# Optimization experiments

Measured on AMD Instinct MI355X. Metric: run time of the kernel, lower is better.

## Reference

```python
import jax, jax.numpy as jnp
from jax import lax
import numpy as np

# pywt.Wavelet('sym5').dec_lo; true convolution with rec_lo == correlation with dec_lo
_DEC_LO = jnp.array([0.027333068345077982, 0.029519490925774643, -0.039134249302383094,
                     0.1993975339773936, 0.7234076904024206, 0.6339789634582119,
                     0.01660210576452232, -0.17532808990845047, -0.021101834024758855,
                     0.019538882735286728], dtype=jnp.float32)
_KERNEL = _DEC_LO[None, None, :]  # (O=1, I=1, L=10)


def _idwt_approx(c):
    # One inverse-DWT level with zero detail coeffs.
    # pywt idwt: upsample by 2, full conv with rec_lo, slice [L-2 : L-2 + 2n-L+2].
    # Equivalent: lhs_dilation=2, padding=(1,1), correlation with dec_lo.
    B, n = c.shape
    out = lax.conv_general_dilated(c[:, None, :], _KERNEL, window_strides=(1,),
                                   padding=[(1, 1)], lhs_dilation=(2,),
                                   dimension_numbers=('NCH', 'OIH', 'NCH'))
    return out[:, 0, :]  # (B, 2n - 8)


def _waverec3(cA):
    # waverec with coeffs [cA(20), zeros(20), zeros(31), zeros(54)], sym5 -> length 100
    a = _idwt_approx(cA)      # 20 -> 32
    a = a[:, :31]             # pywt waverec crops a to len(d)=31
    a = _idwt_approx(a)       # 31 -> 54
    a = _idwt_approx(a)       # 54 -> 100
    return a


def _ce(logits, target):
    logp = jax.nn.log_softmax(logits, axis=-1)
    return -jnp.take_along_axis(logp, target[:, None], axis=-1)[:, 0]


def _ohem(logits, target, train_mask, ratio=3.0):
    ce = _ce(logits, target)
    tf = target.astype(jnp.float32)
    pos = (tf * train_mask) > 0
    neg = ((1.0 - tf) * train_mask) > 0
    n_pos = jnp.sum(pos.astype(jnp.float32))
    count_neg = jnp.sum(neg.astype(jnp.float32))
    loss_pos = jnp.where(n_pos > 0, jnp.sum(jnp.where(pos, ce, 0.0)), 0.0)
    n_neg = jnp.where(n_pos > 0, jnp.minimum(count_neg, jnp.floor(ratio * n_pos)), 100.0)
    srt = jnp.sort(jnp.where(neg, ce, -jnp.inf))[::-1]
    take = (jnp.arange(srt.shape[0]) < n_neg) & jnp.isfinite(srt)
    loss_neg = jnp.sum(jnp.where(take, srt, 0.0))
    return (loss_pos + loss_neg) / (n_pos + n_neg)


def _smooth_l1(d):
    ad = jnp.abs(d)
    return jnp.where(ad < 1.0, 0.5 * d * d, ad - 0.5)


def _forward_single(cls_pred, reg_pred, gt):
    cp = jnp.transpose(cls_pred, (0, 2, 3, 1)).reshape(-1, 4)
    rp = jnp.transpose(reg_pred, (0, 2, 3, 1)).reshape(-1, 42)
    g = jnp.transpose(gt, (0, 2, 3, 1)).reshape(-1, 45)
    tr_pred, tcl_pred = cp[:, :2], cp[:, 2:]
    wl_r, xc_p, wl_i, yc_p = rp[:, :20], rp[:, 20], rp[:, 21:41], rp[:, 41]
    tr_mask, tcl_mask, train_mask = g[:, 0], g[:, 1], g[:, 2]
    real_g, xc_g, imag_g, yc_g = g[:, 3:23], g[:, 23], g[:, 24:44], g[:, 44]
    ttm = train_mask * tr_mask
    n_pos = jnp.sum(ttm)

    loss_tr = _ohem(tr_pred, tr_mask.astype(jnp.int32), train_mask)

    ce_tcl = _ce(tcl_pred, tcl_mask.astype(jnp.int32))
    neg_m = 1.0 - ttm
    mp = jnp.sum(ce_tcl * ttm) / jnp.maximum(n_pos, 1.0)
    mn = jnp.sum(ce_tcl * neg_m) / jnp.maximum(jnp.sum(neg_m), 1.0)
    loss_tcl = jnp.where(n_pos > 0, mp + 0.5 * mn, 0.0)

    px = _waverec3(wl_r) + xc_p[:, None]   # (M,100)
    py = _waverec3(wl_i) + yc_p[:, None]
    gx = _waverec3(real_g) + xc_g[:, None]
    gy = _waverec3(imag_g) + yc_g[:, None]
    per_pix = jnp.sum(_smooth_l1(px - gx) + _smooth_l1(py - gy), axis=-1)  # (M,)
    loss_contour = jnp.where(n_pos > 0, 0.5 * jnp.sum(ttm * per_pix) / (n_pos * 200.0), 0.0)
    return jnp.stack([loss_tr, loss_tcl, loss_contour])


def setup_inputs() -> dict:
    key = jax.random.key(0)
    N = 8
    out = {}
    for name, H in (("3", 100), ("4", 50), ("5", 25)):
        k1, k2, k3, k4, k5, k6 = jax.random.split(jax.random.fold_in(key, int(name)), 6)
        out["cls" + name] = jax.random.normal(k1, (N, 4, H, H), jnp.float32)
        out["reg" + name] = jax.random.normal(k2, (N, 42, H, H), jnp.float32)
        tr = jax.random.bernoulli(k3, 0.1, (N, 1, H, H)).astype(jnp.float32)
        tcl = jax.random.bernoulli(k4, 0.5, (N, 1, H, H)).astype(jnp.float32)
        train = jax.random.bernoulli(k5, 0.9, (N, 1, H, H)).astype(jnp.float32)
        rest = jax.random.normal(k6, (N, 42, H, H), jnp.float32)
        out["gt" + name] = jnp.concatenate([tr, tcl, train, rest], axis=1)  # 45 ch
    return out


def reference(cls3, reg3, gt3, cls4, reg4, gt4, cls5, reg5, gt5):
    total = (_forward_single(cls3, reg3, gt3)
             + _forward_single(cls4, reg4, gt4)
             + _forward_single(cls5, reg5, gt5))
    return total  # [loss_text, loss_center, loss_contour]
```

## Files before the change

kernel.cpp:

```cpp
#include <hip/hip_runtime.h>
#include <math.h>

#define DEVI __device__ __forceinline__

static constexpr float KD[10] = {
  0.027333068345077982f,  0.029519490925774643f, -0.039134249302383094f,
  0.1993975339773936f,    0.7234076904024206f,    0.6339789634582119f,
  0.01660210576452232f,  -0.17532808990845047f,  -0.021101834024758855f,
  0.019538882735286728f};

#define CE_OFF     0
#define PH_OFF     105056
#define PH1_REL    40192
#define PH2_REL    50432
#define MH_OFF     160608
#define BS_OFF     234336
#define SLOTGT_OFF 308064
#define STATE_OFF  308352
#define SLOT2_OFF  308384
#define CBUF_OFF   308672
#define CAPC       49152
#define PART_OFF   456128
#define PART_STRIDE 3840

#define NB3 157
#define NB4 40
#define NB5 20
#define NBR 96

DEVI float wave_sum(float v) {
#pragma unroll
  for (int d = 32; d; d >>= 1) v += __shfl_down(v, d);
  return v;
}

DEVI float block_sum(float v, float* sh) {
  int lane = threadIdx.x & 63, wid = threadIdx.x >> 6;
  v = wave_sum(v);
  if (lane == 0) sh[wid] = v;
  __syncthreads();
  if (threadIdx.x == 0) {
    float s = 0.f;
    int nw = blockDim.x >> 6;
    for (int w = 0; w < nw; ++w) s += sh[w];
    sh[0] = s;
  }
  __syncthreads();
  float r = sh[0];
  __syncthreads();
  return r;
}

DEVI int suffix_scan_256(int v, int* sh) {
  int t = threadIdx.x;
  sh[t] = v;
  __syncthreads();
#pragma unroll
  for (int off = 1; off < 256; off <<= 1) {
    int x = (t + off < 256) ? sh[t + off] : 0;
    __syncthreads();
    sh[t] += x;
    __syncthreads();
  }
  return sh[t];
}

DEVI float sl1(float v) { float a = fabsf(v); return (a < 1.f) ? 0.5f * v * v : a - 0.5f; }

DEVI float ce2cls(float la, float lb, float tgt) {
  float m = fmaxf(la, lb);
  float lse = m + __logf(__expf(la - m) + __expf(lb - m));
  return lse - ((tgt > 0.5f) ? lb : la);
}

template <int H>
DEVI float recon_half(const float* __restrict__ rb, const float* __restrict__ gb,
                      int rc0, int gc0, size_t HW, float off) {
  constexpr int CLO  = (H == 0) ? 0 : 6;
  constexpr int A1LO = (H == 0) ? 0 : 12;
  constexpr int J2LO = (H == 0) ? 0 : 25;
  float c[14];
#pragma unroll
  for (int i = 0; i < 14; ++i)
    c[i] = rb[(size_t)(rc0 + CLO + i) * HW] - gb[(size_t)(gc0 + CLO + i) * HW];
  float a1[19];
#pragma unroll
  for (int k = 0; k < 19; ++k) {
    int o1 = A1LO + k, b = (o1 >> 1) - CLO;
    if (o1 & 1)
      a1[k] = KD[0]*c[b] + KD[2]*c[b+1] + KD[4]*c[b+2] + KD[6]*c[b+3] + KD[8]*c[b+4];
    else
      a1[k] = KD[1]*c[b] + KD[3]*c[b+1] + KD[5]*c[b+2] + KD[7]*c[b+3] + KD[9]*c[b+4];
  }
  float w0=0.f,w1=0.f,w2=0.f,w3=0.f,w4=0.f, acc=0.f;
#pragma unroll
  for (int k = 0; k < 29; ++k) {
    int j2 = J2LO + k, b = (j2 >> 1) - A1LO;
    float a2v;
    if (j2 & 1)
      a2v = KD[0]*a1[b] + KD[2]*a1[b+1] + KD[4]*a1[b+2] + KD[6]*a1[b+3] + KD[8]*a1[b+4];
    else
      a2v = KD[1]*a1[b] + KD[3]*a1[b+1] + KD[5]*a1[b+2] + KD[7]*a1[b+3] + KD[9]*a1[b+4];
    w0=w1; w1=w2; w2=w3; w3=w4; w4=a2v;
    if (k >= 4) {
      acc += sl1(KD[1]*w0 + KD[3]*w1 + KD[5]*w2 + KD[7]*w3 + KD[9]*w4 + off);
      acc += sl1(KD[0]*w0 + KD[2]*w1 + KD[4]*w2 + KD[6]*w3 + KD[8]*w4 + off);
    }
  }
  return acc;
}

DEVI float2 tap2o(const float2* a, int b) {
  float2 r;
  r.x = KD[0]*a[b].x + KD[2]*a[b+1].x + KD[4]*a[b+2].x + KD[6]*a[b+3].x + KD[8]*a[b+4].x;
  r.y = KD[0]*a[b].y + KD[2]*a[b+1].y + KD[4]*a[b+2].y + KD[6]*a[b+3].y + KD[8]*a[b+4].y;
  return r;
}
DEVI float2 tap2e(const float2* a, int b) {
  float2 r;
  r.x = KD[1]*a[b].x + KD[3]*a[b+1].x + KD[5]*a[b+2].x + KD[7]*a[b+3].x + KD[9]*a[b+4].x;
  r.y = KD[1]*a[b].y + KD[3]*a[b+1].y + KD[5]*a[b+2].y + KD[7]*a[b+3].y + KD[9]*a[b+4].y;
  return r;
}
template <int H>
DEVI float2 recon2(const float* __restrict__ rb, const float* __restrict__ gb,
                   int rc0, int gc0, size_t HW, float2 off) {
  constexpr int CLO  = (H == 0) ? 0 : 6;
  constexpr int A1LO = (H == 0) ? 0 : 12;
  constexpr int J2LO = (H == 0) ? 0 : 25;
  float2 c[14];
#pragma unroll
  for (int i = 0; i < 14; ++i) {
    float2 rv = *(const float2*)(rb + (size_t)(rc0 + CLO + i) * HW);
    float2 gv = *(const float2*)(gb + (size_t)(gc0 + CLO + i) * HW);
    c[i].x = rv.x - gv.x; c[i].y = rv.y - gv.y;
  }
  float2 a1[19];
#pragma unroll
  for (int k = 0; k < 19; ++k) {
    int o1 = A1LO + k, b = (o1 >> 1) - CLO;
    a1[k] = (o1 & 1) ? tap2o(c, b) : tap2e(c, b);
  }
  float2 w0={0,0},w1={0,0},w2={0,0},w3={0,0},w4={0,0};
  float2 acc={0,0};
#pragma unroll
  for (int k = 0; k < 29; ++k) {
    int j2 = J2LO + k, b = (j2 >> 1) - A1LO;
    float2 a2v = (j2 & 1) ? tap2o(a1, b) : tap2e(a1, b);
    w0=w1; w1=w2; w2=w3; w3=w4; w4=a2v;
    if (k >= 4) {
      float vex = KD[1]*w0.x + KD[3]*w1.x + KD[5]*w2.x + KD[7]*w3.x + KD[9]*w4.x + off.x;
      float vey = KD[1]*w0.y + KD[3]*w1.y + KD[5]*w2.y + KD[7]*w3.y + KD[9]*w4.y + off.y;
      float vox = KD[0]*w0.x + KD[2]*w1.x + KD[4]*w2.x + KD[6]*w3.x + KD[8]*w4.x + off.x;
      float voy = KD[0]*w0.y + KD[2]*w1.y + KD[4]*w2.y + KD[6]*w3.y + KD[8]*w4.y + off.y;
      acc.x += sl1(vex) + sl1(vox);
      acc.y += sl1(vey) + sl1(voy);
    }
  }
  return acc;
}

__global__ void __launch_bounds__(256, 3)
pixel_kernel(const float* __restrict__ cls3, const float* __restrict__ reg3, const float* __restrict__ gt3,
             const float* __restrict__ cls4, const float* __restrict__ reg4, const float* __restrict__ gt4,
             const float* __restrict__ cls5, const float* __restrict__ reg5, const float* __restrict__ gt5,
             float* __restrict__ ws, float* __restrict__ out) {
  int bx = blockIdx.x, y = blockIdx.y, t = threadIdx.x;
  int axis = y >> 1, half = y & 1;
  const float *cls, *reg, *gt;
  int M, HW, ceOff, partBase, phRel, nb, lbx, two;
  if (bx < NB3) {
    cls = cls3; reg = reg3; gt = gt3; M = 80000; HW = 10000;
    ceOff = 0; partBase = PART_OFF; phRel = 0; nb = NB3; lbx = bx; two = 1;
  } else if (bx < NB3 + NB4) {
    cls = cls4; reg = reg4; gt = gt4; M = 20000; HW = 2500;
    ceOff = 80000; partBase = PART_OFF + PART_STRIDE; phRel = PH1_REL; nb = NB4; lbx = bx - NB3; two = 1;
  } else {
    cls = cls5; reg = reg5; gt = gt5; M = 5000; HW = 625;
    ceOff = 100000; partBase = PART_OFF + 2 * PART_STRIDE; phRel = PH2_REL; nb = NB5; lbx = bx - NB3 - NB4; two = 0;
  }
  float* ceArr = ws + ceOff;
  unsigned* ph = (unsigned*)(ws + PH_OFF) + phRel;

  if (bx == 0 && y == 0 && t < 3) out[t] = 0.f;

  __shared__ unsigned hlds[256];
  __shared__ float shp[4][6];
  hlds[t] = 0u;
  __syncthreads();

  float cnt_pos = 0.f, cnt_neg = 0.f, s_ce_pos = 0.f, s_tcl_ttm = 0.f, s_tcl_negm = 0.f;
  float s_ttm_pp = 0.f;
  int rc0 = axis ? 21 : 0;
  int gc0 = axis ? 24 : 3;

  if (two) {
    int p0 = (lbx * 256 + t) * 2;
    if (p0 < M) {
      int n = p0 / HW, hw = p0 % HW;
      const float* gb = gt  + (size_t)n * 45 * HW + hw;
      const float* rb = reg + (size_t)n * 42 * HW + hw;
      float2 trv = *(const float2*)(gb);
      float2 tnv = *(const float2*)(gb + 2 * (size_t)HW);
      float2 ttm; ttm.x = trv.x * tnv.x; ttm.y = trv.y * tnv.y;

      if (y == 0) {
        const float* cb = cls + (size_t)n * 4 * HW + hw;
        float2 l0 = *(const float2*)(cb);
        float2 l1 = *(const float2*)(cb + (size_t)HW);
        float2 l2 = *(const float2*)(cb + 2 * (size_t)HW);
        float2 l3 = *(const float2*)(cb + 3 * (size_t)HW);
        float2 tcl = *(const float2*)(gb + (size_t)HW);
        float cex = ce2cls(l0.x, l1.x, trv.x), cey = ce2cls(l0.y, l1.y, trv.y);
        float ctx = ce2cls(l2.x, l3.x, tcl.x), cty = ce2cls(l2.y, l3.y, tcl.y);
        bool posx = ttm.x > 0.f, posy = ttm.y > 0.f;
        bool negx = ((1.f - trv.x) * tnv.x) > 0.f, negy = ((1.f - trv.y) * tnv.y) > 0.f;
        float cvx = negx ? cex : 0.f, cvy = negy ? cey : 0.f;
        float2 cev; cev.x = cvx; cev.y = cvy;
        *(float2*)(ceArr + p0) = cev;
        if (negx) atomicAdd(&hlds[__float_as_uint(cvx) >> 23], 1u);
        if (negy) atomicAdd(&hlds[__float_as_uint(cvy) >> 23], 1u);
        cnt_pos = (posx ? 1.f : 0.f) + (posy ? 1.f : 0.f);
        cnt_neg = (negx ? 1.f : 0.f) + (negy ? 1.f : 0.f);
        s_ce_pos = (posx ? cex : 0.f) + (posy ? cey : 0.f);
        s_tcl_ttm = ctx * ttm.x + cty * ttm.y;
        s_tcl_negm = ctx * (1.f - ttm.x) + cty * (1.f - ttm.y);
      }

      float2 rcv = *(const float2*)(rb + (size_t)(rc0 + 20) * HW);
      float2 gcv = *(const float2*)(gb + (size_t)(gc0 + 20) * HW);
      float2 dc; dc.x = rcv.x - gcv.x; dc.y = rcv.y - gcv.y;
      float2 pp = half ? recon2<1>(rb, gb, rc0, gc0, (size_t)HW, dc)
                       : recon2<0>(rb, gb, rc0, gc0, (size_t)HW, dc);
      s_ttm_pp = ttm.x * pp.x + ttm.y * pp.y;
    }
  } else {
    int p = lbx * 256 + t;
    if (p < M) {
      int n = p / HW, hw = p % HW;
      const float* gb = gt  + (size_t)n * 45 * HW + hw;
      const float* rb = reg + (size_t)n * 42 * HW + hw;
      float tr = gb[0], train = gb[2 * (size_t)HW];
      float ttm = tr * train;
      if (y == 0) {
        const float* cb = cls + (size_t)n * 4 * HW + hw;
        float ce_tr = ce2cls(cb[0], cb[(size_t)HW], tr);
        float ce_tcl = ce2cls(cb[2 * (size_t)HW], cb[3 * (size_t)HW], gb[(size_t)HW]);
        bool pos = ttm > 0.f;
        bool neg = ((1.f - tr) * train) > 0.f;
        float cev = neg ? ce_tr : 0.f;
        ceArr[p] = cev;
        if (neg) atomicAdd(&hlds[__float_as_uint(cev) >> 23], 1u);
        cnt_pos = pos ? 1.f : 0.f;
        cnt_neg = neg ? 1.f : 0.f;
        s_ce_pos = pos ? ce_tr : 0.f;
        s_tcl_ttm = ce_tcl * ttm;
        s_tcl_negm = ce_tcl * (1.f - ttm);
      }
      float dc = rb[(size_t)(rc0 + 20) * HW] - gb[(size_t)(gc0 + 20) * HW];
      float pp = half ? recon_half<1>(rb, gb, rc0, gc0, (size_t)HW, dc)
                      : recon_half<0>(rb, gb, rc0, gc0, (size_t)HW, dc);
      s_ttm_pp = ttm * pp;
    }
  }

  int lane = t & 63, wid = t >> 6;
  cnt_pos = wave_sum(cnt_pos);
  cnt_neg = wave_sum(cnt_neg);
  s_ce_pos = wave_sum(s_ce_pos);
  s_tcl_ttm = wave_sum(s_tcl_ttm);
  s_tcl_negm = wave_sum(s_tcl_negm);
  s_ttm_pp = wave_sum(s_ttm_pp);
  if (lane == 0) {
    shp[wid][0] = cnt_pos; shp[wid][1] = cnt_neg; shp[wid][2] = s_ce_pos;
    shp[wid][3] = s_tcl_ttm; shp[wid][4] = s_tcl_negm; shp[wid][5] = s_ttm_pp;
  }
  __syncthreads();
  if (t < 6) {
    float s = shp[0][t] + shp[1][t] + shp[2][t] + shp[3][t];
    ws[partBase + (size_t)(y * nb + lbx) * 6 + t] = s;
  }
  if (y == 0)
    ph[(size_t)lbx * 256 + t] = hlds[t];
}

__global__ void refine_kernel(float* __restrict__ ws) {
  int s = blockIdx.y, r = blockIdx.x, t = threadIdx.x;
  int M   = (s == 0) ? 80000 : (s == 1 ? 20000 : 5000);
  int off = (s == 0) ? 0     : (s == 1 ? 80000 : 100000);
  int nb0 = (s == 0) ? NB3   : (s == 1 ? NB4   : NB5);
  int phRel = (s == 0) ? 0 : (s == 1 ? PH1_REL : PH2_REL);
  int* st = (int*)(ws + STATE_OFF) + s * 8;

  __shared__ int sh[256];
  __shared__ int sel[2];
  __shared__ float red[4];
  __shared__ unsigned hW[4][256];
  __shared__ unsigned mhL[256];
  __shared__ float bsL[256];

  const float* part = ws + PART_OFF + s * PART_STRIDE;
  int npart = 4 * nb0;
  float a0 = 0.f, a1 = 0.f, a2 = 0.f, a3 = 0.f, a4 = 0.f, a5 = 0.f;
  for (int i = t; i < npart; i += 256) {
    const float* p6 = part + (size_t)i * 6;
    a0 += p6[0]; a1 += p6[1]; a2 += p6[2]; a3 += p6[3]; a4 += p6[4]; a5 += p6[5];
  }
  a0 = block_sum(a0, red);
  a1 = block_sum(a1, red);
  a2 = block_sum(a2, red);
  a3 = block_sum(a3, red);
  a4 = block_sum(a4, red);
  a5 = block_sum(a5, red);

  float cnt_pos = a0, cnt_negf = a1;
  int cnt_neg = (int)cnt_negf;
  float kf = (cnt_pos > 0.f) ? fminf(cnt_negf, floorf(3.f * cnt_pos)) : 100.f;
  int k_take = min((int)kf, cnt_neg);

  int ibin, rem;
  if (k_take >= cnt_neg) { ibin = -1; rem = 0; }
  else if (k_take <= 0)  { ibin = 256; rem = 0; }
  else {
    const uint4* ph4 = (const uint4*)((const unsigned*)(ws + PH_OFF) + phRel);
    unsigned c0 = 0u, c1 = 0u, c2 = 0u, c3 = 0u;
    int n4 = nb0 * 64;
    for (int i = t; i < n4; i += 256) {
      uint4 u = ph4[i];
      c0 += u.x; c1 += u.y; c2 += u.z; c3 += u.w;
    }
    int wid = t >> 6, b0 = (4 * t) & 255;
    hW[wid][b0 + 0] = c0; hW[wid][b0 + 1] = c1; hW[wid][b0 + 2] = c2; hW[wid][b0 + 3] = c3;
    __syncthreads();
    int h = (int)(hW[0][t] + hW[1][t] + hW[2][t] + hW[3][t]);
    int suf = suffix_scan_256(h, sh);
    int above = suf - h;
    if (suf >= k_take && above < k_take) { sel[0] = t; sel[1] = k_take - above; }
    __syncthreads();
    ibin = sel[0]; rem = sel[1];
    __syncthreads();
  }
  if (r == 0 && t == 0) {
    st[0] = ibin; st[1] = rem;
    float* stf = (float*)st;
    stf[2] = kf; stf[3] = a0; stf[4] = a2; stf[5] = a3; stf[6] = a4; stf[7] = a5;
  }

  mhL[t] = 0u; bsL[t] = 0.f;
  __syncthreads();
  const float* ce = ws + off;
  float sum = 0.f;
  for (int i = r * 256 + t; i < M; i += NBR * 256) {
    float v = ce[i];
    unsigned b = __float_as_uint(v);
    int e = (int)(b >> 23);
    if (e > ibin) sum += v;
    else if (e == ibin && rem > 0) {
      int m8 = (int)((b >> 15) & 255u);
      atomicAdd(&mhL[m8], 1u);
      atomicAdd(&bsL[m8], v);
    }
  }
  sum = block_sum(sum, red);
  if (t == 0) ws[SLOTGT_OFF + s * NBR + r] = sum;
  if (rem > 0) {
    ((unsigned*)(ws + MH_OFF))[((size_t)s * NBR + r) * 256 + t] = mhL[t];
    ws[BS_OFF + ((size_t)s * NBR + r) * 256 + t] = bsL[t];
  }
}

__global__ void compactB_kernel(float* __restrict__ ws) {
  int s = blockIdx.y, r = blockIdx.x, t = threadIdx.x;
  int M   = (s == 0) ? 80000 : (s == 1 ? 20000 : 5000);
  int off = (s == 0) ? 0     : (s == 1 ? 80000 : 100000);
  const int* st = (const int*)(ws + STATE_OFF) + s * 8;
  int ibin = st[0], rem = st[1];
  if (rem <= 0) return;

  __shared__ int sh[256];
  __shared__ int sel[2];
  __shared__ float red[4];
  __shared__ unsigned hW[4][256];
  __shared__ unsigned wcnt;

  const unsigned* mh = (const unsigned*)(ws + MH_OFF) + (size_t)s * NBR * 256;
  const uint4* mh4 = (const uint4*)mh;
  unsigned c0 = 0u, c1 = 0u, c2 = 0u, c3 = 0u;
  for (int i = t; i < NBR * 64; i += 256) {
    uint4 u = mh4[i];
    c0 += u.x; c1 += u.y; c2 += u.z; c3 += u.w;
  }
  int wid = t >> 6, b0 = (4 * t) & 255;
  hW[wid][b0 + 0] = c0; hW[wid][b0 + 1] = c1; hW[wid][b0 + 2] = c2; hW[wid][b0 + 3] = c3;
  __syncthreads();
  int h = (int)(hW[0][t] + hW[1][t] + hW[2][t] + hW[3][t]);
  int suf = suffix_scan_256(h, sh);
  int above = suf - h;
  if (suf >= rem && above < rem) { sel[0] = t; }
  __syncthreads();
  int jbin = sel[0];
  __syncthreads();

  float v2 = ws[BS_OFF + ((size_t)s * NBR + r) * 256 + t];
  float gt2 = block_sum((t > jbin) ? v2 : 0.f, red);
  if (t == 0) ws[SLOT2_OFF + s * NBR + r] = gt2;

  int cval = (t < NBR) ? (int)mh[(size_t)t * 256 + jbin] : 0;
  sh[t] = cval;
  __syncthreads();
#pragma unroll
  for (int o = 1; o < 128; o <<= 1) {
    int x = (t >= o) ? sh[t - o] : 0;
    __syncthreads();
    sh[t] += x;
    __syncthreads();
  }
  int base = (r > 0) ? sh[r - 1] : 0;

  if (t == 0) wcnt = 0u;
  __syncthreads();
  const float* ce = ws + off;
  float* cbuf = ws + CBUF_OFF + (size_t)s * CAPC;
  for (int i = r * 256 + t; i < M; i += NBR * 256) {
    float v = ce[i];
    unsigned b = __float_as_uint(v);
    if ((int)(b >> 23) == ibin && (int)((b >> 15) & 255u) == jbin) {
      unsigned idx = (unsigned)base + atomicAdd(&wcnt, 1u);
      if (idx < CAPC) cbuf[idx] = v;
    }
  }
}

__global__ void final_kernel(float* __restrict__ ws, float* __restrict__ out) {
  int s = blockIdx.x, t = threadIdx.x;
  int M = (s == 0) ? 80000 : (s == 1 ? 20000 : 5000);
  const int* st = (const int*)(ws + STATE_OFF) + s * 8;
  const float* stf = (const float*)st;

  __shared__ int sh[256];
  __shared__ int sel[2];
  __shared__ float red[4];
  __shared__ unsigned hW[4][256];
  __shared__ int hist[256];

  int ibin = st[0], rem = st[1];
  float kf = stf[2], n_pos = stf[3];
  float s_ce_pos = stf[4], s_tcl_ttm = stf[5], s_tcl_negm = stf[6], s_ttm_pp = stf[7];

  float lpart = (t < NBR) ? ws[SLOTGT_OFF + s * NBR + t] : 0.f;
  float loss_neg = block_sum(lpart, red);

  if (rem > 0) {
    const uint4* mh4 = (const uint4*)((const unsigned*)(ws + MH_OFF) + (size_t)s * NBR * 256);
    unsigned c0 = 0u, c1 = 0u, c2 = 0u, c3 = 0u;
    for (int i = t; i < NBR * 64; i += 256) {
      uint4 u = mh4[i];
      c0 += u.x; c1 += u.y; c2 += u.z; c3 += u.w;
    }
    int wid = t >> 6, b0 = (4 * t) & 255;
    hW[wid][b0 + 0] = c0; hW[wid][b0 + 1] = c1; hW[wid][b0 + 2] = c2; hW[wid][b0 + 3] = c3;
    __syncthreads();
    int h = (int)(hW[0][t] + hW[1][t] + hW[2][t] + hW[3][t]);
    int suf = suffix_scan_256(h, sh);
    int above = suf - h;
    if (suf >= rem && above < rem) { sel[0] = t; sel[1] = rem - above; }
    __syncthreads();
    int jbin = sel[0], rem2 = sel[1];
    int jcnt = (int)(hW[0][jbin] + hW[1][jbin] + hW[2][jbin] + hW[3][jbin]);
    __syncthreads();

    float l2 = (t < NBR) ? ws[SLOT2_OFF + s * NBR + t] : 0.f;
    loss_neg += block_sum(l2, red);

    int cnt = min(jcnt, CAPC);
    const float* cbuf = ws + CBUF_OFF + (size_t)s * CAPC;

    hist[t] = 0; __syncthreads();
    for (int i = t; i < cnt; i += 256)
      atomicAdd(&hist[(__float_as_uint(cbuf[i]) >> 7) & 255u], 1);
    __syncthreads();
    h = hist[t];
    suf = suffix_scan_256(h, sh);
    above = suf - h;
    int remcur = rem2;
    if (suf >= remcur && above < remcur) { sel[0] = t; sel[1] = remcur - above; }
    __syncthreads();
    int b1 = sel[0]; remcur = sel[1];
    __syncthreads();

    hist[t] = 0; __syncthreads();
    for (int i = t; i < cnt; i += 256) {
      unsigned b = __float_as_uint(cbuf[i]);
      if (((b >> 7) & 255u) == (unsigned)b1) atomicAdd(&hist[b & 127u], 1);
    }
    __syncthreads();
    h = (t < 128) ? hist[t] : 0;
    suf = suffix_scan_256(h, sh);
    above = suf - h;
    if (t < 128 && suf >= remcur && above < remcur) { sel[0] = t; }
    __syncthreads();
    int lb0 = sel[0];
    __syncthreads();

    unsigned prefix = ((unsigned)ibin << 23) | ((unsigned)jbin << 15) |
                      ((unsigned)b1 << 7) | (unsigned)lb0;
    float tval = __uint_as_float(prefix);

    float sum_in = 0.f, cgt = 0.f;
    for (int i = t; i < cnt; i += 256) {
      unsigned b = __float_as_uint(cbuf[i]);
      if (b > prefix) { sum_in += cbuf[i]; cgt += 1.f; }
    }
    sum_in = block_sum(sum_in, red);
    cgt = block_sum(cgt, red);
    loss_neg += sum_in + ((float)rem2 - cgt) * tval;
  }

  if (t == 0) {
    float loss_pos = (n_pos > 0.f) ? s_ce_pos : 0.f;
    float loss_tr = (loss_pos + loss_neg) / (n_pos + kf);

    float negm = (float)M - n_pos;
    float mp = s_tcl_ttm / fmaxf(n_pos, 1.f);
    float mn = s_tcl_negm / fmaxf(negm, 1.f);
    float loss_tcl = (n_pos > 0.f) ? (mp + 0.5f * mn) : 0.f;

    float loss_ct = (n_pos > 0.f) ? (0.5f * s_ttm_pp / (n_pos * 200.f)) : 0.f;

    atomicAdd(&out[0], loss_tr);
    atomicAdd(&out[1], loss_tcl);
    atomicAdd(&out[2], loss_ct);
  }
}

extern "C" void kernel_launch(void* const* d_in, const int* in_sizes, int n_in,
                              void* d_out, int out_size, void* d_ws, size_t ws_size,
                              hipStream_t stream) {
  (void)in_sizes; (void)n_in; (void)out_size; (void)ws_size;
  const float* cls3 = (const float*)d_in[0];
  const float* reg3 = (const float*)d_in[1];
  const float* gt3  = (const float*)d_in[2];
  const float* cls4 = (const float*)d_in[3];
  const float* reg4 = (const float*)d_in[4];
  const float* gt4  = (const float*)d_in[5];
  const float* cls5 = (const float*)d_in[6];
  const float* reg5 = (const float*)d_in[7];
  const float* gt5  = (const float*)d_in[8];

  float* ws = (float*)d_ws;
  float* out = (float*)d_out;

  pixel_kernel<<<dim3(NB3 + NB4 + NB5, 4), 256, 0, stream>>>(
      cls3, reg3, gt3, cls4, reg4, gt4, cls5, reg5, gt5, ws, out);

  refine_kernel<<<dim3(NBR, 3), 256, 0, stream>>>(ws);
  compactB_kernel<<<dim3(NBR, 3), 256, 0, stream>>>(ws);
  final_kernel<<<3, 256, 0, stream>>>(ws, out);
}
```

Measured before the change: 58.52 us.

## Compute full wavelet reconstruction per thread with streaming windows instead of halves

Replaces the two half-reconstruction blocks per axis with one block per axis that computes all three inverse-DWT levels in a single pass. Level-1 and level-2 outputs are kept in five-register sliding windows instead of full arrays. This removes the overlapping halo work and the duplicated gt/ttm loads that the two halves repeated, and halves the grid's y dimension. The occupancy hint rises from 3 to 4 blocks per SIMD. In exchange each thread does more serial work and there are fewer blocks to hide latency.

After: 90.27 us. 54.3% more time.

```diff
diff --git a/kernel.cpp b/kernel.cpp
--- a/kernel.cpp
+++ b/kernel.cpp
@@ -73,100 +73,101 @@
   return lse - ((tgt > 0.5f) ? lb : la);
 }
 
-template <int H>
-DEVI float recon_half(const float* __restrict__ rb, const float* __restrict__ gb,
+DEVI float recon_full(const float* __restrict__ rb, const float* __restrict__ gb,
                       int rc0, int gc0, size_t HW, float off) {
-  constexpr int CLO  = (H == 0) ? 0 : 6;
-  constexpr int A1LO = (H == 0) ? 0 : 12;
-  constexpr int J2LO = (H == 0) ? 0 : 25;
-  float c[14];
-#pragma unroll
-  for (int i = 0; i < 14; ++i)
-    c[i] = rb[(size_t)(rc0 + CLO + i) * HW] - gb[(size_t)(gc0 + CLO + i) * HW];
-  float a1[19];
-#pragma unroll
-  for (int k = 0; k < 19; ++k) {
-    int o1 = A1LO + k, b = (o1 >> 1) - CLO;
-    if (o1 & 1)
-      a1[k] = KD[0]*c[b] + KD[2]*c[b+1] + KD[4]*c[b+2] + KD[6]*c[b+3] + KD[8]*c[b+4];
+  float c[20];
+#pragma unroll
+  for (int i = 0; i < 20; ++i)
+    c[i] = rb[(size_t)(rc0 + i) * HW] - gb[(size_t)(gc0 + i) * HW];
+  float a1w0=0.f,a1w1=0.f,a1w2=0.f,a1w3=0.f,a1w4=0.f;
+  float a2w0=0.f,a2w1=0.f,a2w2=0.f,a2w3=0.f,a2w4=0.f;
+  float acc = 0.f;
+#pragma unroll
+  for (int j1 = 0; j1 < 31; ++j1) {
+    int b = j1 >> 1;
+    float a1v;
+    if (j1 & 1)
+      a1v = KD[0]*c[b] + KD[2]*c[b+1] + KD[4]*c[b+2] + KD[6]*c[b+3] + KD[8]*c[b+4];
     else
-      a1[k] = KD[1]*c[b] + KD[3]*c[b+1] + KD[5]*c[b+2] + KD[7]*c[b+3] + KD[9]*c[b+4];
-  }
-  float w0=0.f,w1=0.f,w2=0.f,w3=0.f,w4=0.f, acc=0.f;
-#pragma unroll
-  for (int k = 0; k < 29; ++k) {
-    int j2 = J2LO + k, b = (j2 >> 1) - A1LO;
-    float a2v;
-    if (j2 & 1)
-      a2v = KD[0]*a1[b] + KD[2]*a1[b+1] + KD[4]*a1[b+2] + KD[6]*a1[b+3] + KD[8]*a1[b+4];
-    else
-      a2v = KD[1]*a1[b] + KD[3]*a1[b+1] + KD[5]*a1[b+2] + KD[7]*a1[b+3] + KD[9]*a1[b+4];
-    w0=w1; w1=w2; w2=w3; w3=w4; w4=a2v;
-    if (k >= 4) {
-      acc += sl1(KD[1]*w0 + KD[3]*w1 + KD[5]*w2 + KD[7]*w3 + KD[9]*w4 + off);
-      acc += sl1(KD[0]*w0 + KD[2]*w1 + KD[4]*w2 + KD[6]*w3 + KD[8]*w4 + off);
+      a1v = KD[1]*c[b] + KD[3]*c[b+1] + KD[5]*c[b+2] + KD[7]*c[b+3] + KD[9]*c[b+4];
+    a1w0=a1w1; a1w1=a1w2; a1w2=a1w3; a1w3=a1w4; a1w4=a1v;
+    if (j1 >= 4) {
+#pragma unroll
+      for (int tt = 0; tt < 2; ++tt) {
+        float a2v;
+        if (tt)
+          a2v = KD[0]*a1w0 + KD[2]*a1w1 + KD[4]*a1w2 + KD[6]*a1w3 + KD[8]*a1w4;
+        else
+          a2v = KD[1]*a1w0 + KD[3]*a1w1 + KD[5]*a1w2 + KD[7]*a1w3 + KD[9]*a1w4;
+        a2w0=a2w1; a2w1=a2w2; a2w2=a2w3; a2w3=a2w4; a2w4=a2v;
+        int j2 = 2 * (j1 - 4) + tt;
+        if (j2 >= 4) {
+          acc += sl1(KD[1]*a2w0 + KD[3]*a2w1 + KD[5]*a2w2 + KD[7]*a2w3 + KD[9]*a2w4 + off);
+          acc += sl1(KD[0]*a2w0 + KD[2]*a2w1 + KD[4]*a2w2 + KD[6]*a2w3 + KD[8]*a2w4 + off);
+        }
+      }
     }
   }
   return acc;
 }
 
-DEVI float2 tap2o(const float2* a, int b) {
-  float2 r;
-  r.x = KD[0]*a[b].x + KD[2]*a[b+1].x + KD[4]*a[b+2].x + KD[6]*a[b+3].x + KD[8]*a[b+4].x;
-  r.y = KD[0]*a[b].y + KD[2]*a[b+1].y + KD[4]*a[b+2].y + KD[6]*a[b+3].y + KD[8]*a[b+4].y;
-  return r;
-}
-DEVI float2 tap2e(const float2* a, int b) {
-  float2 r;
-  r.x = KD[1]*a[b].x + KD[3]*a[b+1].x + KD[5]*a[b+2].x + KD[7]*a[b+3].x + KD[9]*a[b+4].x;
-  r.y = KD[1]*a[b].y + KD[3]*a[b+1].y + KD[5]*a[b+2].y + KD[7]*a[b+3].y + KD[9]*a[b+4].y;
-  return r;
-}
-template <int H>
-DEVI float2 recon2(const float* __restrict__ rb, const float* __restrict__ gb,
-                   int rc0, int gc0, size_t HW, float2 off) {
-  constexpr int CLO  = (H == 0) ? 0 : 6;
-  constexpr int A1LO = (H == 0) ? 0 : 12;
-  constexpr int J2LO = (H == 0) ? 0 : 25;
-  float2 c[14];
-#pragma unroll
-  for (int i = 0; i < 14; ++i) {
-    float2 rv = *(const float2*)(rb + (size_t)(rc0 + CLO + i) * HW);
-    float2 gv = *(const float2*)(gb + (size_t)(gc0 + CLO + i) * HW);
+DEVI float2 recon2_full(const float* __restrict__ rb, const float* __restrict__ gb,
+                        int rc0, int gc0, size_t HW, float2 off) {
+  float2 c[20];
+#pragma unroll
+  for (int i = 0; i < 20; ++i) {
+    float2 rv = *(const float2*)(rb + (size_t)(rc0 + i) * HW);
+    float2 gv = *(const float2*)(gb + (size_t)(gc0 + i) * HW);
     c[i].x = rv.x - gv.x; c[i].y = rv.y - gv.y;
   }
-  float2 a1[19];
-#pragma unroll
-  for (int k = 0; k < 19; ++k) {
-    int o1 = A1LO + k, b = (o1 >> 1) - CLO;
-    a1[k] = (o1 & 1) ? tap2o(c, b) : tap2e(c, b);
-  }
-  float2 w0={0,0},w1={0,0},w2={0,0},w3={0,0},w4={0,0};
+  float2 a1w0={0,0},a1w1={0,0},a1w2={0,0},a1w3={0,0},a1w4={0,0};
+  float2 a2w0={0,0},a2w1={0,0},a2w2={0,0},a2w3={0,0},a2w4={0,0};
   float2 acc={0,0};
 #pragma unroll
-  for (int k = 0; k < 29; ++k) {
-    int j2 = J2LO + k, b = (j2 >> 1) - A1LO;
-    float2 a2v = (j2 & 1) ? tap2o(a1, b) : tap2e(a1, b);
-    w0=w1; w1=w2; w2=w3; w3=w4; w4=a2v;
-    if (k >= 4) {
-      float vex = KD[1]*w0.x + KD[3]*w1.x + KD[5]*w2.x + KD[7]*w3.x + KD[9]*w4.x + off.x;
-      float vey = KD[1]*w0.y + KD[3]*w1.y + KD[5]*w2.y + KD[7]*w3.y + KD[9]*w4.y + off.y;
-      float vox = KD[0]*w0.x + KD[2]*w1.x + KD[4]*w2.x + KD[6]*w3.x + KD[8]*w4.x + off.x;
-      float voy = KD[0]*w0.y + KD[2]*w1.y + KD[4]*w2.y + KD[6]*w3.y + KD[8]*w4.y + off.y;
-      acc.x += sl1(vex) + sl1(vox);
-      acc.y += sl1(vey) + sl1(voy);
+  for (int j1 = 0; j1 < 31; ++j1) {
+    int b = j1 >> 1;
+    float2 a1v;
+    if (j1 & 1) {
+      a1v.x = KD[0]*c[b].x + KD[2]*c[b+1].x + KD[4]*c[b+2].x + KD[6]*c[b+3].x + KD[8]*c[b+4].x;
+      a1v.y = KD[0]*c[b].y + KD[2]*c[b+1].y + KD[4]*c[b+2].y + KD[6]*c[b+3].y + KD[8]*c[b+4].y;
+    } else {
+      a1v.x = KD[1]*c[b].x + KD[3]*c[b+1].x + KD[5]*c[b+2].x + KD[7]*c[b+3].x + KD[9]*c[b+4].x;
+      a1v.y = KD[1]*c[b].y + KD[3]*c[b+1].y + KD[5]*c[b+2].y + KD[7]*c[b+3].y + KD[9]*c[b+4].y;
+    }
+    a1w0=a1w1; a1w1=a1w2; a1w2=a1w3; a1w3=a1w4; a1w4=a1v;
+    if (j1 >= 4) {
+#pragma unroll
+      for (int tt = 0; tt < 2; ++tt) {
+        float2 a2v;
+        if (tt) {
+          a2v.x = KD[0]*a1w0.x + KD[2]*a1w1.x + KD[4]*a1w2.x + KD[6]*a1w3.x + KD[8]*a1w4.x;
+          a2v.y = KD[0]*a1w0.y + KD[2]*a1w1.y + KD[4]*a1w2.y + KD[6]*a1w3.y + KD[8]*a1w4.y;
+        } else {
+          a2v.x = KD[1]*a1w0.x + KD[3]*a1w1.x + KD[5]*a1w2.x + KD[7]*a1w3.x + KD[9]*a1w4.x;
+          a2v.y = KD[1]*a1w0.y + KD[3]*a1w1.y + KD[5]*a1w2.y + KD[7]*a1w3.y + KD[9]*a1w4.y;
+        }
+        a2w0=a2w1; a2w1=a2w2; a2w2=a2w3; a2w3=a2w4; a2w4=a2v;
+        int j2 = 2 * (j1 - 4) + tt;
+        if (j2 >= 4) {
+          float vex = KD[1]*a2w0.x + KD[3]*a2w1.x + KD[5]*a2w2.x + KD[7]*a2w3.x + KD[9]*a2w4.x + off.x;
+          float vey = KD[1]*a2w0.y + KD[3]*a2w1.y + KD[5]*a2w2.y + KD[7]*a2w3.y + KD[9]*a2w4.y + off.y;
+          float vox = KD[0]*a2w0.x + KD[2]*a2w1.x + KD[4]*a2w2.x + KD[6]*a2w3.x + KD[8]*a2w4.x + off.x;
+          float voy = KD[0]*a2w0.y + KD[2]*a2w1.y + KD[4]*a2w2.y + KD[6]*a2w3.y + KD[8]*a2w4.y + off.y;
+          acc.x += sl1(vex) + sl1(vox);
+          acc.y += sl1(vey) + sl1(voy);
+        }
+      }
     }
   }
   return acc;
 }
 
-__global__ void __launch_bounds__(256, 3)
+__global__ void __launch_bounds__(256, 4)
 pixel_kernel(const float* __restrict__ cls3, const float* __restrict__ reg3, const float* __restrict__ gt3,
              const float* __restrict__ cls4, const float* __restrict__ reg4, const float* __restrict__ gt4,
              const float* __restrict__ cls5, const float* __restrict__ reg5, const float* __restrict__ gt5,
              float* __restrict__ ws, float* __restrict__ out) {
-  int bx = blockIdx.x, y = blockIdx.y, t = threadIdx.x;
-  int axis = y >> 1, half = y & 1;
+  int bx = blockIdx.x, axis = blockIdx.y, t = threadIdx.x;
   const float *cls, *reg, *gt;
   int M, HW, ceOff, partBase, phRel, nb, lbx, two;
   if (bx < NB3) {
@@ -182,7 +183,7 @@
   float* ceArr = ws + ceOff;
   unsigned* ph = (unsigned*)(ws + PH_OFF) + phRel;
 
-  if (bx == 0 && y == 0 && t < 3) out[t] = 0.f;
+  if (bx == 0 && axis == 0 && t < 3) out[t] = 0.f;
 
   __shared__ unsigned hlds[256];
   __shared__ float shp[4][6];
@@ -204,7 +205,7 @@
       float2 tnv = *(const float2*)(gb + 2 * (size_t)HW);
       float2 ttm; ttm.x = trv.x * tnv.x; ttm.y = trv.y * tnv.y;
 
-      if (y == 0) {
+      if (axis == 0) {
         const float* cb = cls + (size_t)n * 4 * HW + hw;
         float2 l0 = *(const float2*)(cb);
         float2 l1 = *(const float2*)(cb + (size_t)HW);
@@ -230,8 +231,7 @@
       float2 rcv = *(const float2*)(rb + (size_t)(rc0 + 20) * HW);
       float2 gcv = *(const float2*)(gb + (size_t)(gc0 + 20) * HW);
       float2 dc; dc.x = rcv.x - gcv.x; dc.y = rcv.y - gcv.y;
-      float2 pp = half ? recon2<1>(rb, gb, rc0, gc0, (size_t)HW, dc)
-                       : recon2<0>(rb, gb, rc0, gc0, (size_t)HW, dc);
+      float2 pp = recon2_full(rb, gb, rc0, gc0, (size_t)HW, dc);
       s_ttm_pp = ttm.x * pp.x + ttm.y * pp.y;
     }
   } else {
@@ -242,7 +242,7 @@
       const float* rb = reg + (size_t)n * 42 * HW + hw;
       float tr = gb[0], train = gb[2 * (size_t)HW];
       float ttm = tr * train;
-      if (y == 0) {
+      if (axis == 0) {
         const float* cb = cls + (size_t)n * 4 * HW + hw;
         float ce_tr = ce2cls(cb[0], cb[(size_t)HW], tr);
         float ce_tcl = ce2cls(cb[2 * (size_t)HW], cb[3 * (size_t)HW], gb[(size_t)HW]);
@@ -258,8 +258,7 @@
         s_tcl_negm = ce_tcl * (1.f - ttm);
       }
       float dc = rb[(size_t)(rc0 + 20) * HW] - gb[(size_t)(gc0 + 20) * HW];
-      float pp = half ? recon_half<1>(rb, gb, rc0, gc0, (size_t)HW, dc)
-                      : recon_half<0>(rb, gb, rc0, gc0, (size_t)HW, dc);
+      float pp = recon_full(rb, gb, rc0, gc0, (size_t)HW, dc);
       s_ttm_pp = ttm * pp;
     }
   }
@@ -278,9 +277,9 @@
   __syncthreads();
   if (t < 6) {
     float s = shp[0][t] + shp[1][t] + shp[2][t] + shp[3][t];
-    ws[partBase + (size_t)(y * nb + lbx) * 6 + t] = s;
-  }
-  if (y == 0)
+    ws[partBase + (size_t)(axis * nb + lbx) * 6 + t] = s;
+  }
+  if (axis == 0)
     ph[(size_t)lbx * 256 + t] = hlds[t];
 }
 
@@ -300,7 +299,7 @@
   __shared__ float bsL[256];
 
   const float* part = ws + PART_OFF + s * PART_STRIDE;
-  int npart = 4 * nb0;
+  int npart = 2 * nb0;
   float a0 = 0.f, a1 = 0.f, a2 = 0.f, a3 = 0.f, a4 = 0.f, a5 = 0.f;
   for (int i = t; i < npart; i += 256) {
     const float* p6 = part + (size_t)i * 6;
@@ -550,7 +549,7 @@
   float* ws = (float*)d_ws;
   float* out = (float*)d_out;
 
-  pixel_kernel<<<dim3(NB3 + NB4 + NB5, 4), 256, 0, stream>>>(
+  pixel_kernel<<<dim3(NB3 + NB4 + NB5, 2), 256, 0, stream>>>(
       cls3, reg3, gt3, cls4, reg4, gt4, cls5, reg5, gt5, ws, out);
 
   refine_kernel<<<dim3(NBR, 3), 256, 0, stream>>>(ws);
```
